# Optimization experiments

Hardware: AMD Instinct MI355X
Metric: run time of the kernel (lower is better)

Reference implementation:

```python
import jax, jax.numpy as jnp
import numpy as np

B, C, H, W = 8, 320, 32, 32
HEADS, DHEAD = 8, 40
CTX_LEN, CTX_DIM = 77, 768
FF_INNER = 4 * C
GROUPS = 32
HW = H * W


def setup_inputs() -> dict:
    key = jax.random.key(0)
    ks = jax.random.split(key, 16)
    def nrm(k, shape, s=0.02):
        return (jax.random.normal(k, shape) * s).astype(jnp.float32)
    z = lambda *s: jnp.zeros(s, jnp.float32)
    o = lambda *s: jnp.ones(s, jnp.float32)
    inp = {}
    inp["x"] = jax.random.normal(ks[0], (B, C, H, W), jnp.float32)
    inp["context"] = jax.random.normal(ks[1], (B, CTX_LEN, CTX_DIM), jnp.float32)
    inp["vis_mask"] = jax.random.uniform(ks[2], (B, HW, HW)) > 0.5
    inp["v2t_mask"] = jax.random.uniform(ks[3], (B, HW, CTX_LEN)) > 0.5
    inp["gn_scale"] = o(C); inp["gn_bias"] = z(C)
    inp["proj_in_w"] = nrm(ks[4], (C, C)); inp["proj_in_b"] = z(C)
    inp["n1_s"] = o(C); inp["n1_b"] = z(C)
    inp["wq1"] = nrm(ks[5], (C, C)); inp["wk1"] = nrm(ks[6], (C, C)); inp["wv1"] = nrm(ks[7], (C, C))
    inp["wo1"] = nrm(ks[8], (C, C)); inp["bo1"] = z(C)
    inp["n2_s"] = o(C); inp["n2_b"] = z(C)
    inp["wq2"] = nrm(ks[9], (C, C)); inp["wk2"] = nrm(ks[10], (CTX_DIM, C)); inp["wv2"] = nrm(ks[11], (CTX_DIM, C))
    inp["wo2"] = nrm(ks[12], (C, C)); inp["bo2"] = z(C)
    inp["n3_s"] = o(C); inp["n3_b"] = z(C)
    inp["ff_w1"] = nrm(ks[13], (C, 2 * FF_INNER)); inp["ff_b1"] = z(2 * FF_INNER)
    inp["ff_w2"] = nrm(ks[14], (FF_INNER, C)); inp["ff_b2"] = z(C)
    inp["proj_out_w"] = nrm(ks[15], (C, C)); inp["proj_out_b"] = z(C)
    return inp


def group_norm(x, scale, bias, eps=1e-6):
    b, c, h, w = x.shape
    xg = x.reshape(b, GROUPS, -1)
    mu = xg.mean(-1, keepdims=True)
    var = xg.var(-1, keepdims=True)
    xn = ((xg - mu) * jax.lax.rsqrt(var + eps)).reshape(b, c, h, w)
    return xn * scale[None, :, None, None] + bias[None, :, None, None]


def layer_norm(x, s, b, eps=1e-5):
    mu = x.mean(-1, keepdims=True)
    var = x.var(-1, keepdims=True)
    return (x - mu) * jax.lax.rsqrt(var + eps) * s + b


def mha(xq, ctx, wq, wk, wv, wo, bo, mask):
    # CrossAttention: manual einsum softmax with boolean mask broadcast over heads
    b, n, _ = xq.shape
    m = ctx.shape[1]
    split = lambda t: t.reshape(b, -1, HEADS, DHEAD).transpose(0, 2, 1, 3)
    q = split(xq @ wq)   # [b,h,n,d]
    k = split(ctx @ wk)  # [b,h,m,d]
    v = split(ctx @ wv)
    sim = jnp.einsum('bhid,bhjd->bhij', q, k) * (DHEAD ** -0.5)
    if mask is not None:
        sim = jnp.where(mask[:, None, :, :], sim, jnp.finfo(sim.dtype).min)
    attn = jax.nn.softmax(sim, axis=-1)
    out = jnp.einsum('bhij,bhjd->bhid', attn, v)
    out = out.transpose(0, 2, 1, 3).reshape(b, n, HEADS * DHEAD)
    return out @ wo + bo


def reference(x, context, vis_mask, v2t_mask, gn_scale, gn_bias, proj_in_w, proj_in_b,
              n1_s, n1_b, wq1, wk1, wv1, wo1, bo1,
              n2_s, n2_b, wq2, wk2, wv2, wo2, bo2,
              n3_s, n3_b, ff_w1, ff_b1, ff_w2, ff_b2,
              proj_out_w, proj_out_b):
    x_in = x
    h = group_norm(x, gn_scale, gn_bias)
    # 1x1 conv proj_in == per-pixel linear; flatten b c h w -> b (hw) c
    h = h.reshape(B, C, HW).transpose(0, 2, 1) @ proj_in_w + proj_in_b
    # masked self-attention (vis mask)
    h = h + mha(layer_norm(h, n1_s, n1_b), layer_norm(h, n1_s, n1_b),
                wq1, wk1, wv1, wo1, bo1, vis_mask)
    # masked cross-attention to text (v2t mask)
    h = h + mha(layer_norm(h, n2_s, n2_b), context,
                wq2, wk2, wv2, wo2, bo2, v2t_mask)
    # GEGLU feedforward (glu=True, mult=4)
    y = layer_norm(h, n3_s, n3_b) @ ff_w1 + ff_b1
    a, g = jnp.split(y, 2, axis=-1)
    h = h + (a * jax.nn.gelu(g, approximate=False)) @ ff_w2 + ff_b2
    # proj_out + residual
    out = (h @ proj_out_w + proj_out_b).transpose(0, 2, 1).reshape(B, C, H, W)
    return out + x_in
```

## Files before the change

kernel.cpp:

```cpp
#include <hip/hip_runtime.h>
#include <hip/hip_bf16.h>
#include <math.h>


#define Bsz   8
#define Cch   320
#define HW    1024
#define NTOK  (Bsz*HW)
#define HEADS 8
#define DHEAD 40
#define CTXL  77
#define CTXD  768
#define FFI   1280
#define MCTX  (Bsz*CTXL)
#define MCTXP 640

typedef unsigned short u16;
typedef unsigned long long u64;
typedef __attribute__((ext_vector_type(8))) u16    u16x8;
typedef __attribute__((ext_vector_type(8))) __bf16 bf16x8;
typedef __attribute__((ext_vector_type(4))) float  f32x4;

__device__ inline u16 f2b(float f) {
    unsigned u = __float_as_uint(f);
    return (u16)((u + 0x7FFFu + ((u >> 16) & 1u)) >> 16);
}

__global__ __launch_bounds__(256) void gn_apply(
    const float* __restrict__ x, const float* __restrict__ gnA,
    const float* __restrict__ gnB, u16* __restrict__ out)
{
    __shared__ u16 T[64*72];
    const int tid = threadIdx.x;
    const int c0 = blockIdx.x * 64;
    const int p0 = blockIdx.y * 64;
    const int b  = blockIdx.z;
    for (int e = tid; e < 512; e += 256) {
        int r = e >> 3, ch = e & 7;
        const float* src = x + ((size_t)(b*Cch + c0 + r))*HW + p0 + ch*8;
        float a  = gnA[b*Cch + c0 + r];
        float bb = gnB[b*Cch + c0 + r];
        float4 v0 = *(const float4*)src;
        float4 v1 = *(const float4*)(src + 4);
        u16x8 val;
        val[0] = f2b(v0.x*a + bb); val[1] = f2b(v0.y*a + bb);
        val[2] = f2b(v0.z*a + bb); val[3] = f2b(v0.w*a + bb);
        val[4] = f2b(v1.x*a + bb); val[5] = f2b(v1.y*a + bb);
        val[6] = f2b(v1.z*a + bb); val[7] = f2b(v1.w*a + bb);
        *(u16x8*)&T[r*72 + (ch ^ (r & 7))*8] = val;
    }
    __syncthreads();
    for (int e = tid; e < 4096; e += 256) {
        int p = e >> 6, c = e & 63;
        u16 v = T[c*72 + (((p >> 3) ^ (c & 7))*8) + (p & 7)];
        out[((size_t)(b*HW + p0 + p))*Cch + c0 + c] = v;
    }
}

__global__ __launch_bounds__(256) void layernorm_kernel(
    const float* __restrict__ in, const float* __restrict__ s,
    const float* __restrict__ bgain, u16* __restrict__ out)
{
    int t = blockIdx.x*4 + (threadIdx.x >> 6);
    int lane = threadIdx.x & 63;
    const float* row = in + (size_t)t*Cch;
    float v[5];
    float sum = 0.f, sq = 0.f;
    #pragma unroll
    for (int i = 0; i < 5; ++i) {
        v[i] = row[lane + 64*i];
        sum += v[i]; sq += v[i]*v[i];
    }
    #pragma unroll
    for (int off = 32; off > 0; off >>= 1) {
        sum += __shfl_xor(sum, off);
        sq  += __shfl_xor(sq,  off);
    }
    float mean = sum * (1.f/320.f);
    float var  = sq  * (1.f/320.f) - mean*mean;
    float inv  = rsqrtf(var + 1e-5f);
    u16* orow = out + (size_t)t*Cch;
    #pragma unroll
    for (int i = 0; i < 5; ++i) {
        int c = lane + 64*i;
        orow[c] = f2b((v[i]-mean)*inv*s[c] + bgain[c]);
    }
}

struct WDesc { const float* src; u16* dst; int K; int N; int tiles; float scl; };
struct WPack { WDesc w[12]; };

#define WT_TILES 620
#define CTXBLK   240

__global__ __launch_bounds__(256) void preamble(
    WPack p, const float* __restrict__ ctxsrc, u16* __restrict__ ctxdst,
    const void* __restrict__ vis, const void* __restrict__ v2t,
    u64* __restrict__ bvis, u64* __restrict__ bv2t,
    const float* __restrict__ x, const float* __restrict__ gscale,
    const float* __restrict__ gbias, float* __restrict__ gnA,
    float* __restrict__ gnB)
{
    __shared__ u16 T[64*72];
    int blk = blockIdx.x;
    int tid = threadIdx.x;
    if (blk < WT_TILES) {
        int t = blk;
        #pragma unroll
        for (int i = 0; i < 12; ++i) {
            int nt = p.w[i].tiles;
            if (t < nt) {
                const int K = p.w[i].K, N = p.w[i].N;
                const int ntN = N >> 6;
                const int tk = t / ntN, tn = t - tk*ntN;
                const float scl = p.w[i].scl;
                const float* src = p.w[i].src;
                u16* dst = p.w[i].dst;
                for (int e = tid; e < 512; e += 256) {
                    int r = e >> 3, ch = e & 7;
                    const float* sp = src + (size_t)(tk*64 + r)*N + tn*64 + ch*8;
                    float4 v0 = *(const float4*)sp;
                    float4 v1 = *(const float4*)(sp + 4);
                    u16x8 val;
                    val[0] = f2b(v0.x*scl); val[1] = f2b(v0.y*scl);
                    val[2] = f2b(v0.z*scl); val[3] = f2b(v0.w*scl);
                    val[4] = f2b(v1.x*scl); val[5] = f2b(v1.y*scl);
                    val[6] = f2b(v1.z*scl); val[7] = f2b(v1.w*scl);
                    *(u16x8*)&T[r*72 + (ch ^ (r & 7))*8] = val;
                }
                __syncthreads();
                for (int e = tid; e < 4096; e += 256) {
                    int n = e >> 6, k = e & 63;
                    u16 v = T[k*72 + (((n >> 3) ^ (k & 7))*8) + (n & 7)];
                    dst[(size_t)(tn*64 + n)*K + tk*64 + k] = v;
                }
                return;
            }
            t -= nt;
        }
        return;
    }
    if (blk < WT_TILES + CTXBLK) {
        int idx = (blk - WT_TILES)*2048 + tid*8;
        int r = idx / CTXD;
        u16x8 val = {};
        if (r < MCTX) {
            float4 v0 = *(const float4*)(ctxsrc + idx);
            float4 v1 = *(const float4*)(ctxsrc + idx + 4);
            val[0] = f2b(v0.x); val[1] = f2b(v0.y);
            val[2] = f2b(v0.z); val[3] = f2b(v0.w);
            val[4] = f2b(v1.x); val[5] = f2b(v1.y);
            val[6] = f2b(v1.z); val[7] = f2b(v1.w);
        }
        *(u16x8*)(ctxdst + idx) = val;
        return;
    }
    if (blk >= WT_TILES + CTXBLK + 4096) {
        int gb = blk - (WT_TILES + CTXBLK + 4096);
        int b = gb >> 5, g = gb & 31;
        __shared__ float rs[256], rq[256];
        const float4* xg = (const float4*)(x + ((size_t)b*Cch + g*10)*HW);
        float s = 0.f, q = 0.f;
        #pragma unroll
        for (int i = 0; i < 10; ++i) {
            float4 v = xg[tid + i*256];
            s += v.x + v.y + v.z + v.w;
            q += v.x*v.x + v.y*v.y + v.z*v.z + v.w*v.w;
        }
        rs[tid] = s; rq[tid] = q; __syncthreads();
        for (int off = 128; off > 0; off >>= 1) {
            if (tid < off) { rs[tid] += rs[tid+off]; rq[tid] += rq[tid+off]; }
            __syncthreads();
        }
        if (tid < 10) {
            float mean = rs[0] * (1.f/10240.f);
            float var  = rq[0] * (1.f/10240.f) - mean*mean;
            float inv  = rsqrtf(var + 1e-6f);
            int chn = g*10 + tid;
            float a = inv * gscale[chn];
            gnA[b*Cch + chn] = a;
            gnB[b*Cch + chn] = gbias[chn] - mean*a;
        }
        return;
    }
    __shared__ int any;
    if (tid == 0) any = 0;
    __syncthreads();
    const unsigned char* probe = (const unsigned char*)vis;
    for (int i = tid; i < 4096; i += 256)
        if ((i & 3) && probe[i]) any = 1;
    __syncthreads();
    const int isU8 = any;
    int mb = blk - WT_TILES - CTXBLK;
    const void* mask; u64* bits; int Lkv, nw;
    if (mb < 2048) { mask = vis; bits = bvis; Lkv = HW;   nw = 16; }
    else           { mask = v2t; bits = bv2t; Lkv = CTXL; nw = 2; mb -= 2048; }
    const int wv = tid >> 6, lane = tid & 63;
    const int row = mb*4 + wv;
    const unsigned char* m8  = (const unsigned char*)mask;
    const int*           m32 = (const int*)mask;
    const size_t base = (size_t)row * Lkv;
    for (int w = 0; w < nw; ++w) {
        int j = w*64 + lane;
        bool on = (j < Lkv) && (isU8 ? (m8[base+j] != 0) : (m32[base+j] != 0));
        u64 word = __ballot(on);
        if (lane == 0) bits[(size_t)row*nw + w] = word;
    }
}

__global__ __launch_bounds__(512) void gemm_bf16(
    const u16* __restrict__ A, const u16* __restrict__ Wt,
    const float* __restrict__ bias, const float* __restrict__ res,
    float* __restrict__ out, u16* __restrict__ out_bf, int M, int N, int K)
{
    __shared__ u16 As[2][128*40];
    __shared__ u16 Bs[2][64*40];
    const int tid  = threadIdx.x;
    const int lane = tid & 63;
    const int w    = tid >> 6;
    const int mp   = w >> 1;
    const int np   = w & 1;
    const int m0   = blockIdx.y * 128;
    const int n0   = blockIdx.x * 64;
    const int fr   = lane & 15, fg = lane >> 4;
    const int ar   = tid >> 2, ac = tid & 3;
    const bool hasB = tid < 256;

    const u16* pa = A  + (size_t)(m0 + ar)*K + ac*8;
    const u16* pb = Wt + (size_t)(n0 + ar)*K + ac*8;
    const int nk = K >> 5;

    *(u16x8*)&As[0][ar*40 + ac*8] = *(const u16x8*)pa;
    if (hasB) *(u16x8*)&Bs[0][ar*40 + ac*8] = *(const u16x8*)pb;
    u16x8 xa = *(const u16x8*)(pa + 32);
    u16x8 ya = *(const u16x8*)(pa + 64);
    u16x8 xb = {}, yb = {};
    if (hasB) { xb = *(const u16x8*)(pb + 32); yb = *(const u16x8*)(pb + 64); }

    f32x4 acc[2][2] = {};
    for (int i = 0; i < nk; i += 2) {
        __syncthreads();
        *(u16x8*)&As[1][ar*40 + ac*8] = xa;
        if (hasB) *(u16x8*)&Bs[1][ar*40 + ac*8] = xb;
        if (i + 3 < nk) {
            xa = *(const u16x8*)(pa + 32*(i+3));
            if (hasB) xb = *(const u16x8*)(pb + 32*(i+3));
        }
        {
            bf16x8 a0 = *(const bf16x8*)&As[0][(mp*32      + fr)*40 + fg*8];
            bf16x8 a1 = *(const bf16x8*)&As[0][(mp*32 + 16 + fr)*40 + fg*8];
            #pragma unroll
            for (int t = 0; t < 2; ++t) {
                bf16x8 b = *(const bf16x8*)&Bs[0][((np*2+t)*16 + fr)*40 + fg*8];
                acc[0][t] = __builtin_amdgcn_mfma_f32_16x16x32_bf16(a0, b, acc[0][t], 0, 0, 0);
                acc[1][t] = __builtin_amdgcn_mfma_f32_16x16x32_bf16(a1, b, acc[1][t], 0, 0, 0);
            }
        }
        __syncthreads();
        if (i + 2 < nk) {
            *(u16x8*)&As[0][ar*40 + ac*8] = ya;
            if (hasB) *(u16x8*)&Bs[0][ar*40 + ac*8] = yb;
            if (i + 4 < nk) {
                ya = *(const u16x8*)(pa + 32*(i+4));
                if (hasB) yb = *(const u16x8*)(pb + 32*(i+4));
            }
        }
        {
            bf16x8 a0 = *(const bf16x8*)&As[1][(mp*32      + fr)*40 + fg*8];
            bf16x8 a1 = *(const bf16x8*)&As[1][(mp*32 + 16 + fr)*40 + fg*8];
            #pragma unroll
            for (int t = 0; t < 2; ++t) {
                bf16x8 b = *(const bf16x8*)&Bs[1][((np*2+t)*16 + fr)*40 + fg*8];
                acc[0][t] = __builtin_amdgcn_mfma_f32_16x16x32_bf16(a0, b, acc[0][t], 0, 0, 0);
                acc[1][t] = __builtin_amdgcn_mfma_f32_16x16x32_bf16(a1, b, acc[1][t], 0, 0, 0);
            }
        }
    }
    #pragma unroll
    for (int at = 0; at < 2; ++at) {
        #pragma unroll
        for (int t = 0; t < 2; ++t) {
            int gn = n0 + (np*2+t)*16 + fr;
            float bv = bias ? bias[gn] : 0.f;
            #pragma unroll
            for (int i = 0; i < 4; ++i) {
                int gm = m0 + mp*32 + at*16 + fg*4 + i;
                float v = acc[at][t][i] + bv;
                if (res) v += res[(size_t)gm*N + gn];
                if (out) out[(size_t)gm*N + gn] = v;
                if (out_bf) out_bf[(size_t)gm*N + gn] = f2b(v);
            }
        }
    }
}

__global__ __launch_bounds__(512) void gemm_pout(
    const u16* __restrict__ A, const u16* __restrict__ Wt,
    const float* __restrict__ bias, const float* __restrict__ x,
    float* __restrict__ out, int K)
{
    __shared__ u16 As[2][128*40];
    __shared__ u16 Bs[2][64*40];
    const int tid  = threadIdx.x;
    const int lane = tid & 63;
    const int w    = tid >> 6;
    const int mp   = w >> 1;
    const int np   = w & 1;
    const int m0   = blockIdx.y * 128;
    const int n0   = blockIdx.x * 64;
    const int fr   = lane & 15, fg = lane >> 4;
    const int ar   = tid >> 2, ac = tid & 3;
    const bool hasB = tid < 256;

    const u16* pa = A  + (size_t)(m0 + ar)*K + ac*8;
    const u16* pb = Wt + (size_t)(n0 + ar)*K + ac*8;
    const int nk = K >> 5;

    *(u16x8*)&As[0][ar*40 + ac*8] = *(const u16x8*)pa;
    if (hasB) *(u16x8*)&Bs[0][ar*40 + ac*8] = *(const u16x8*)pb;
    u16x8 xa = *(const u16x8*)(pa + 32);
    u16x8 ya = *(const u16x8*)(pa + 64);
    u16x8 xb = {}, yb = {};
    if (hasB) { xb = *(const u16x8*)(pb + 32); yb = *(const u16x8*)(pb + 64); }

    f32x4 acc[2][2] = {};
    for (int i = 0; i < nk; i += 2) {
        __syncthreads();
        *(u16x8*)&As[1][ar*40 + ac*8] = xa;
        if (hasB) *(u16x8*)&Bs[1][ar*40 + ac*8] = xb;
        if (i + 3 < nk) {
            xa = *(const u16x8*)(pa + 32*(i+3));
            if (hasB) xb = *(const u16x8*)(pb + 32*(i+3));
        }
        {
            bf16x8 a0 = *(const bf16x8*)&As[0][(mp*32      + fr)*40 + fg*8];
            bf16x8 a1 = *(const bf16x8*)&As[0][(mp*32 + 16 + fr)*40 + fg*8];
            #pragma unroll
            for (int t = 0; t < 2; ++t) {
                bf16x8 b = *(const bf16x8*)&Bs[0][((np*2+t)*16 + fr)*40 + fg*8];
                acc[0][t] = __builtin_amdgcn_mfma_f32_16x16x32_bf16(a0, b, acc[0][t], 0, 0, 0);
                acc[1][t] = __builtin_amdgcn_mfma_f32_16x16x32_bf16(a1, b, acc[1][t], 0, 0, 0);
            }
        }
        __syncthreads();
        if (i + 2 < nk) {
            *(u16x8*)&As[0][ar*40 + ac*8] = ya;
            if (hasB) *(u16x8*)&Bs[0][ar*40 + ac*8] = yb;
            if (i + 4 < nk) {
                ya = *(const u16x8*)(pa + 32*(i+4));
                if (hasB) yb = *(const u16x8*)(pb + 32*(i+4));
            }
        }
        {
            bf16x8 a0 = *(const bf16x8*)&As[1][(mp*32      + fr)*40 + fg*8];
            bf16x8 a1 = *(const bf16x8*)&As[1][(mp*32 + 16 + fr)*40 + fg*8];
            #pragma unroll
            for (int t = 0; t < 2; ++t) {
                bf16x8 b = *(const bf16x8*)&Bs[1][((np*2+t)*16 + fr)*40 + fg*8];
                acc[0][t] = __builtin_amdgcn_mfma_f32_16x16x32_bf16(a0, b, acc[0][t], 0, 0, 0);
                acc[1][t] = __builtin_amdgcn_mfma_f32_16x16x32_bf16(a1, b, acc[1][t], 0, 0, 0);
            }
        }
    }
    #pragma unroll
    for (int at = 0; at < 2; ++at) {
        #pragma unroll
        for (int t = 0; t < 2; ++t) {
            int gn = n0 + (np*2+t)*16 + fr;
            float bv = bias[gn];
            int gm0 = m0 + mp*32 + at*16 + fg*4;
            int b   = gm0 >> 10;
            int pcol= gm0 & (HW-1);
            size_t o = ((size_t)(b*Cch + gn))*HW + pcol;
            f32x4 xv = *(const f32x4*)&x[o];
            f32x4 vv;
            #pragma unroll
            for (int i = 0; i < 4; ++i) vv[i] = acc[at][t][i] + bv + xv[i];
            *(f32x4*)&out[o] = vv;
        }
    }
}

__global__ __launch_bounds__(512) void ctx_kv_gemm(
    const u16* __restrict__ ctx, const u16* __restrict__ wk,
    const u16* __restrict__ wv, u16* __restrict__ kout, u16* __restrict__ vout)
{
    __shared__ u16 As[2][64*40];
    __shared__ u16 Bs[2][64*40];
    const int tid  = threadIdx.x;
    const int lane = tid & 63;
    const int w    = tid >> 6;
    const int mg   = w >> 1;
    const int np   = w & 1;
    const int m0   = blockIdx.y * 64;
    const int n0   = blockIdx.x * 64;
    const u16* Wt  = blockIdx.z ? wv : wk;
    u16* outp      = blockIdx.z ? vout : kout;
    const int fr   = lane & 15, fg = lane >> 4;
    const bool isA = tid < 256;
    const int cr   = (tid & 255) >> 2, cc = tid & 3;

    const u16* ps = isA ? ctx + (size_t)(m0 + cr)*CTXD + cc*8
                        : Wt  + (size_t)(n0 + cr)*CTXD + cc*8;
    u16* s0 = isA ? &As[0][cr*40 + cc*8] : &Bs[0][cr*40 + cc*8];
    u16* s1 = isA ? &As[1][cr*40 + cc*8] : &Bs[1][cr*40 + cc*8];
    const int nk = CTXD >> 5;

    *(u16x8*)s0 = *(const u16x8*)ps;
    u16x8 xv = *(const u16x8*)(ps + 32);
    u16x8 yv = *(const u16x8*)(ps + 64);

    f32x4 acc[2] = {};
    for (int i = 0; i < nk; i += 2) {
        __syncthreads();
        *(u16x8*)s1 = xv;
        if (i + 3 < nk) xv = *(const u16x8*)(ps + 32*(i+3));
        {
            bf16x8 a = *(const bf16x8*)&As[0][(mg*16 + fr)*40 + fg*8];
            #pragma unroll
            for (int t = 0; t < 2; ++t) {
                bf16x8 b = *(const bf16x8*)&Bs[0][((np*2+t)*16 + fr)*40 + fg*8];
                acc[t] = __builtin_amdgcn_mfma_f32_16x16x32_bf16(a, b, acc[t], 0, 0, 0);
            }
        }
        __syncthreads();
        if (i + 2 < nk) {
            *(u16x8*)s0 = yv;
            if (i + 4 < nk) yv = *(const u16x8*)(ps + 32*(i+4));
        }
        {
            bf16x8 a = *(const bf16x8*)&As[1][(mg*16 + fr)*40 + fg*8];
            #pragma unroll
            for (int t = 0; t < 2; ++t) {
                bf16x8 b = *(const bf16x8*)&Bs[1][((np*2+t)*16 + fr)*40 + fg*8];
                acc[t] = __builtin_amdgcn_mfma_f32_16x16x32_bf16(a, b, acc[t], 0, 0, 0);
            }
        }
    }
    #pragma unroll
    for (int t = 0; t < 2; ++t) {
        int gn = n0 + (np*2+t)*16 + fr;
        #pragma unroll
        for (int i = 0; i < 4; ++i) {
            int gm = m0 + mg*16 + fg*4 + i;
            if (gm < MCTX)
                outp[(size_t)gm*Cch + gn] = f2b(acc[t][i]);
        }
    }
}

__global__ __launch_bounds__(512) void geglu_bf16(
    const u16* __restrict__ A, const u16* __restrict__ Wt,
    const float* __restrict__ b1, u16* __restrict__ out, int M, int K)
{
    __shared__ u16 As[2][128*40];
    __shared__ u16 Ba[2][64*40];
    __shared__ u16 Bg[2][64*40];
    const int tid  = threadIdx.x;
    const int lane = tid & 63;
    const int w    = tid >> 6;
    const int mp   = w >> 1;
    const int np   = w & 1;
    const int m0   = blockIdx.y * 128;
    const int n0   = blockIdx.x * 64;
    const int fr   = lane & 15, fg = lane >> 4;
    const int ar   = tid >> 2, ac = tid & 3;
    const int nk   = K >> 5;

    const u16* pa = A + (size_t)(m0 + ar)*K + ac*8;
    const int bq = (ar < 64) ? (n0 + ar) : (FFI + n0 + ar - 64);
    const u16* pb = Wt + (size_t)bq*K + ac*8;
    u16* bs0 = (ar < 64) ? &Ba[0][ar*40 + ac*8] : &Bg[0][(ar-64)*40 + ac*8];
    u16* bs1 = (ar < 64) ? &Ba[1][ar*40 + ac*8] : &Bg[1][(ar-64)*40 + ac*8];

    *(u16x8*)&As[0][ar*40 + ac*8] = *(const u16x8*)pa;
    *(u16x8*)bs0 = *(const u16x8*)pb;
    u16x8 xa = *(const u16x8*)(pa + 32);
    u16x8 xb = *(const u16x8*)(pb + 32);
    u16x8 ya = *(const u16x8*)(pa + 64);
    u16x8 yb = *(const u16x8*)(pb + 64);

    f32x4 aca[2][2] = {}, acg[2][2] = {};
    for (int i = 0; i < nk; i += 2) {
        __syncthreads();
        *(u16x8*)&As[1][ar*40 + ac*8] = xa;
        *(u16x8*)bs1 = xb;
        if (i + 3 < nk) {
            xa = *(const u16x8*)(pa + 32*(i+3));
            xb = *(const u16x8*)(pb + 32*(i+3));
        }
        {
            bf16x8 a0 = *(const bf16x8*)&As[0][(mp*32      + fr)*40 + fg*8];
            bf16x8 a1 = *(const bf16x8*)&As[0][(mp*32 + 16 + fr)*40 + fg*8];
            #pragma unroll
            for (int t = 0; t < 2; ++t) {
                bf16x8 ba = *(const bf16x8*)&Ba[0][((np*2+t)*16 + fr)*40 + fg*8];
                bf16x8 bg = *(const bf16x8*)&Bg[0][((np*2+t)*16 + fr)*40 + fg*8];
                aca[0][t] = __builtin_amdgcn_mfma_f32_16x16x32_bf16(a0, ba, aca[0][t], 0, 0, 0);
                aca[1][t] = __builtin_amdgcn_mfma_f32_16x16x32_bf16(a1, ba, aca[1][t], 0, 0, 0);
                acg[0][t] = __builtin_amdgcn_mfma_f32_16x16x32_bf16(a0, bg, acg[0][t], 0, 0, 0);
                acg[1][t] = __builtin_amdgcn_mfma_f32_16x16x32_bf16(a1, bg, acg[1][t], 0, 0, 0);
            }
        }
        __syncthreads();
        if (i + 2 < nk) {
            *(u16x8*)&As[0][ar*40 + ac*8] = ya;
            *(u16x8*)bs0 = yb;
            if (i + 4 < nk) {
                ya = *(const u16x8*)(pa + 32*(i+4));
                yb = *(const u16x8*)(pb + 32*(i+4));
            }
        }
        {
            bf16x8 a0 = *(const bf16x8*)&As[1][(mp*32      + fr)*40 + fg*8];
            bf16x8 a1 = *(const bf16x8*)&As[1][(mp*32 + 16 + fr)*40 + fg*8];
            #pragma unroll
            for (int t = 0; t < 2; ++t) {
                bf16x8 ba = *(const bf16x8*)&Ba[1][((np*2+t)*16 + fr)*40 + fg*8];
                bf16x8 bg = *(const bf16x8*)&Bg[1][((np*2+t)*16 + fr)*40 + fg*8];
                aca[0][t] = __builtin_amdgcn_mfma_f32_16x16x32_bf16(a0, ba, aca[0][t], 0, 0, 0);
                aca[1][t] = __builtin_amdgcn_mfma_f32_16x16x32_bf16(a1, ba, aca[1][t], 0, 0, 0);
                acg[0][t] = __builtin_amdgcn_mfma_f32_16x16x32_bf16(a0, bg, acg[0][t], 0, 0, 0);
                acg[1][t] = __builtin_amdgcn_mfma_f32_16x16x32_bf16(a1, bg, acg[1][t], 0, 0, 0);
            }
        }
    }
    #pragma unroll
    for (int at = 0; at < 2; ++at) {
        #pragma unroll
        for (int t = 0; t < 2; ++t) {
            int gn = n0 + (np*2+t)*16 + fr;
            float ba = b1[gn], bg = b1[FFI + gn];
            #pragma unroll
            for (int i = 0; i < 4; ++i) {
                int gm = m0 + mp*32 + at*16 + fg*4 + i;
                float av = aca[at][t][i] + ba;
                float gv = acg[at][t][i] + bg;
                float gel = 0.5f*gv*(1.f + erff(gv*0.70710678118654752f));
                out[(size_t)gm*FFI + gn] = f2b(av*gel);
            }
        }
    }
}

__global__ __launch_bounds__(256) void transpose_v(
    const u16* __restrict__ in, int istride, u16* __restrict__ out,
    int Ltok, int ostride)
{
    __shared__ u16 T[64*72];
    const int tid = threadIdx.x;
    const int c0 = blockIdx.x * 64;
    const int t0 = blockIdx.y * 64;
    const int b  = blockIdx.z;
    for (int e = tid; e < 512; e += 256) {
        int r = e >> 3, ch = e & 7;
        u16x8 val = {};
        if (t0 + r < Ltok)
            val = *(const u16x8*)(in + ((size_t)(b*Ltok + t0 + r))*istride + c0 + ch*8);
        *(u16x8*)&T[r*72 + (ch ^ (r & 7))*8] = val;
    }
    __syncthreads();
    for (int e = tid; e < 4096; e += 256) {
        int c = e >> 6, t = e & 63;
        u16 v = T[t*72 + (((c >> 3) ^ (t & 7))*8) + (c & 7)];
        out[((size_t)(b*Cch + c0 + c))*ostride + t0 + t] = v;
    }
}

__global__ __launch_bounds__(256) void flash_mfma(
    const u16* __restrict__ qb, int qstride,
    const u16* __restrict__ kb, int kstride,
    const u16* __restrict__ vt, int vstride,
    const u64* __restrict__ mbits, int nw,
    u16* __restrict__ out,
    int Lkv)
{
    __shared__ u16 QPs[64*72];
    __shared__ u16 Ks[64*72];
    __shared__ u16 Vs[48*72];

    const int tid  = threadIdx.x;
    const int lane = tid & 63;
    const int w    = tid >> 6;
    const int col  = lane & 15;
    const int quad = lane >> 4;
    const int q0   = blockIdx.x * 64;
    const int h    = blockIdx.y;
    const int b    = blockIdx.z;
    const int ch   = tid & 7;
    const int r0   = tid >> 3;

    {
        const u16* qT = qb + ((size_t)(b*HW + q0))*qstride + (size_t)h*DHEAD + ch*8;
        u16x8 v0 = {}, v1 = {};
        if (ch < 5) {
            v0 = *(const u16x8*)(qT + (size_t)r0*qstride);
            v1 = *(const u16x8*)(qT + (size_t)(r0+32)*qstride);
        }
        *(u16x8*)&QPs[r0*72 + ch*8]      = v0;
        *(u16x8*)&QPs[(r0+32)*72 + ch*8] = v1;
    }
    if (tid >= 64 && tid < 128) {
        int dc = 32 + (tid >> 3);
        u16x8 v = {};
        if (dc == DHEAD) {
            #pragma unroll
            for (int z = 0; z < 8; ++z) v[z] = 0x3F80;
        }
        *(u16x8*)&Vs[dc*72 + ch*8] = v;
    }

    const bool kok = ch < 5;
    const u16* kR0 = kb + (size_t)b*Lkv*kstride + (size_t)h*DHEAD + ch*8
                        + (size_t)r0*kstride;
    const u16* kR1 = kR0 + (size_t)32*kstride;
    const int d1   = 32 + (tid >> 3);
    const u16* vR0 = vt + ((size_t)(b*Cch + h*DHEAD))*vstride + ch*8
                        + (size_t)r0*vstride;
    const u16* vR1 = vt + ((size_t)(b*Cch + h*DHEAD))*vstride + ch*8
                        + (size_t)d1*vstride;
    const u64* mrow = mbits + ((size_t)(b*HW + q0 + w*16 + quad*4))*nw;
    const bool vok1 = tid < 64;

    u16x8 nk0 = {}, nk1 = {}, nv0, nv1 = {};
    if (kok && (r0      < Lkv)) nk0 = *(const u16x8*)kR0;
    if (kok && (r0 + 32 < Lkv)) nk1 = *(const u16x8*)kR1;
    nv0 = *(const u16x8*)vR0;
    if (vok1) nv1 = *(const u16x8*)vR1;

    __syncthreads();
    const bf16x8 qa0 = *(const bf16x8*)&QPs[(w*16 + col)*72 +  0 + quad*8];
    const bf16x8 qa1 = *(const bf16x8*)&QPs[(w*16 + col)*72 + 32 + quad*8];

    f32x4 acc_o[3] = {};

    const int nkt = (Lkv + 63) / 64;
    for (int jt = 0; jt < nkt; ++jt) {
        __syncthreads();
        *(u16x8*)&Ks[r0*72 + ch*8]      = nk0;
        *(u16x8*)&Ks[(r0+32)*72 + ch*8] = nk1;
        *(u16x8*)&Vs[r0*72 + ch*8]      = nv0;
        if (vok1) *(u16x8*)&Vs[d1*72 + ch*8] = nv1;
        if (jt + 1 < nkt) {
            const int j0n = (jt + 1)*64;
            kR0 += (size_t)64*kstride;
            kR1 += (size_t)64*kstride;
            vR0 += 64; vR1 += 64;
            nk0 = (u16x8){}; nk1 = (u16x8){};
            if (kok && (j0n + r0      < Lkv)) nk0 = *(const u16x8*)kR0;
            if (kok && (j0n + r0 + 32 < Lkv)) nk1 = *(const u16x8*)kR1;
            nv0 = *(const u16x8*)vR0;
            if (vok1) nv1 = *(const u16x8*)vR1;
        }
        __syncthreads();

        u64 mw[4];
        #pragma unroll
        for (int i = 0; i < 4; ++i) mw[i] = mrow[i*nw + jt];

        f32x4 s[4] = {};
        #pragma unroll
        for (int nt = 0; nt < 4; ++nt) {
            bf16x8 b0 = *(const bf16x8*)&Ks[(nt*16 + col)*72 +  0 + quad*8];
            bf16x8 b1 = *(const bf16x8*)&Ks[(nt*16 + col)*72 + 32 + quad*8];
            s[nt] = __builtin_amdgcn_mfma_f32_16x16x32_bf16(qa0, b0, s[nt], 0, 0, 0);
            s[nt] = __builtin_amdgcn_mfma_f32_16x16x32_bf16(qa1, b1, s[nt], 0, 0, 0);
        }

        #pragma unroll
        for (int i = 0; i < 4; ++i) {
            #pragma unroll
            for (int nt = 0; nt < 4; ++nt) {
                float p = __builtin_amdgcn_exp2f(s[nt][i]);
                unsigned bits = (unsigned)(mw[i] >> (nt*16));
                s[nt][i] = ((bits >> col) & 1u) ? p : 0.f;
            }
        }

        #pragma unroll
        for (int nt = 0; nt < 4; ++nt)
            #pragma unroll
            for (int i = 0; i < 4; ++i)
                QPs[(w*16 + quad*4 + i)*68 + nt*16 + col] =
                    (u16)(__float_as_uint(s[nt][i]) >> 16);

        bf16x8 pa0, pa1;
        __builtin_memcpy(&pa0, &QPs[(w*16 + col)*68 +  0 + quad*8], 16);
        __builtin_memcpy(&pa1, &QPs[(w*16 + col)*68 + 32 + quad*8], 16);
        #pragma unroll
        for (int nt = 0; nt < 3; ++nt) {
            bf16x8 vb0 = *(const bf16x8*)&Vs[(nt*16 + col)*72 +  0 + quad*8];
            bf16x8 vb1 = *(const bf16x8*)&Vs[(nt*16 + col)*72 + 32 + quad*8];
            acc_o[nt] = __builtin_amdgcn_mfma_f32_16x16x32_bf16(pa0, vb0, acc_o[nt], 0, 0, 0);
            acc_o[nt] = __builtin_amdgcn_mfma_f32_16x16x32_bf16(pa1, vb1, acc_o[nt], 0, 0, 0);
        }
    }

    float inv_l[4];
    #pragma unroll
    for (int i = 0; i < 4; ++i)
        inv_l[i] = 1.f / __shfl(acc_o[2][i], (lane & 48) | 8);

    #pragma unroll
    for (int nt = 0; nt < 3; ++nt) {
        int d = nt*16 + col;
        if (d < DHEAD) {
            #pragma unroll
            for (int i = 0; i < 4; ++i) {
                int q = q0 + w*16 + quad*4 + i;
                out[((size_t)(b*HW + q))*Cch + h*DHEAD + d] = f2b(acc_o[nt][i] * inv_l[i]);
            }
        }
    }
}

extern "C" void kernel_launch(void* const* d_in, const int* in_sizes, int n_in,
                              void* d_out, int out_size, void* d_ws, size_t ws_size,
                              hipStream_t stream)
{
    const float* x        = (const float*)d_in[0];
    const float* context  = (const float*)d_in[1];
    const void*  vis_mask = d_in[2];
    const void*  v2t_mask = d_in[3];
    const float* gn_s     = (const float*)d_in[4];
    const float* gn_b     = (const float*)d_in[5];
    const float* proj_in_w= (const float*)d_in[6];
    const float* proj_in_b= (const float*)d_in[7];
    const float* n1_s     = (const float*)d_in[8];
    const float* n1_b     = (const float*)d_in[9];
    const float* wq1      = (const float*)d_in[10];
    const float* wk1      = (const float*)d_in[11];
    const float* wv1      = (const float*)d_in[12];
    const float* wo1      = (const float*)d_in[13];
    const float* bo1      = (const float*)d_in[14];
    const float* n2_s     = (const float*)d_in[15];
    const float* n2_b     = (const float*)d_in[16];
    const float* wq2      = (const float*)d_in[17];
    const float* wk2      = (const float*)d_in[18];
    const float* wv2      = (const float*)d_in[19];
    const float* wo2      = (const float*)d_in[20];
    const float* bo2      = (const float*)d_in[21];
    const float* n3_s     = (const float*)d_in[22];
    const float* n3_b     = (const float*)d_in[23];
    const float* ff_w1    = (const float*)d_in[24];
    const float* ff_b1    = (const float*)d_in[25];
    const float* ff_w2    = (const float*)d_in[26];
    const float* ff_b2    = (const float*)d_in[27];
    const float* pout_w   = (const float*)d_in[28];
    const float* pout_b   = (const float*)d_in[29];
    float* out = (float*)d_out;

    const size_t TOKC = (size_t)NTOK*Cch;
    float* ws   = (float*)d_ws;
    float* Hb   = ws;
    u16*   QKV  = (u16*)(Hb + TOKC);
    u16*   Vt_g = QKV + 3*TOKC;
    u16*   G_bf = QKV;
    u16*   T0b  = Vt_g + TOKC;
    u16*   T1b  = T0b + TOKC;
    u16*   Hb_bf= T1b + TOKC;
    u16*   Wbf  = Hb_bf + TOKC;
    u64*   mb_vis = (u64*)(Wbf + 2539520);
    u64*   mb_v2t = mb_vis + 131072;
    u16*   ctx_bf = (u16*)(mb_v2t + 16384);
    u16*   Kc_bf  = ctx_bf + MCTXP*CTXD;
    u16*   Vc_bf  = Kc_bf + 640*Cch;
    float* gnA    = (float*)(Vc_bf + 640*Cch);
    float* gnB    = gnA + Bsz*Cch;

    u16* w_q1  = Wbf;
    u16* w_k1  = Wbf +  102400;
    u16* w_v1  = Wbf +  204800;
    u16* w_pin = Wbf +  307200;
    u16* w_o1  = Wbf +  409600;
    u16* w_q2  = Wbf +  512000;
    u16* w_o2  = Wbf +  614400;
    u16* w_ff1 = Wbf +  716800;
    u16* w_ff2 = Wbf + 1536000;
    u16* w_po  = Wbf + 1945600;
    u16* w_k2  = Wbf + 2048000;
    u16* w_v2  = Wbf + 2293760;

    const float qscale = 0.15811388300841897f * 1.4426950408889634f;
    WPack pack;
    pack.w[0]  = { wq1,       w_q1,  Cch, Cch, 25,  qscale };
    pack.w[1]  = { wk1,       w_k1,  Cch, Cch, 25,  1.f };
    pack.w[2]  = { wv1,       w_v1,  Cch, Cch, 25,  1.f };
    pack.w[3]  = { proj_in_w, w_pin, Cch, Cch, 25,  1.f };
    pack.w[4]  = { wo1,       w_o1,  Cch, Cch, 25,  1.f };
    pack.w[5]  = { wq2,       w_q2,  Cch, Cch, 25,  qscale };
    pack.w[6]  = { wo2,       w_o2,  Cch, Cch, 25,  1.f };
    pack.w[7]  = { ff_w1,     w_ff1, Cch, 2*FFI, 200, 1.f };
    pack.w[8]  = { ff_w2,     w_ff2, FFI, Cch, 100, 1.f };
    pack.w[9]  = { pout_w,    w_po,  Cch, Cch, 25,  1.f };
    pack.w[10] = { wk2,       w_k2,  CTXD, Cch, 60, 1.f };
    pack.w[11] = { wv2,       w_v2,  CTXD, Cch, 60, 1.f };

    dim3 blk256(256);
    dim3 blk512(512);
    dim3 gTok(Cch/64, NTOK/128);
    dim3 gQKV(960/64, NTOK/128);
    dim3 gKV(Cch/64, MCTXP/64, 2);
    dim3 gFF(FFI/64, NTOK/128);
    dim3 gFA(HW/64, HEADS, Bsz);
    dim3 gTrS(Cch/64, HW/64, Bsz);
    dim3 gTrX(Cch/64, 2, Bsz);
    dim3 gGN(Cch/64, HW/64, Bsz);

    preamble<<<WT_TILES + CTXBLK + 4096 + 256, blk256, 0, stream>>>(
        pack, context, ctx_bf, vis_mask, v2t_mask, mb_vis, mb_v2t,
        x, gn_s, gn_b, gnA, gnB);

    gn_apply<<<gGN, blk256, 0, stream>>>(x, gnA, gnB, T0b);
    gemm_bf16<<<gTok, blk512, 0, stream>>>(T0b, w_pin, proj_in_b, nullptr, Hb, nullptr, NTOK, Cch, Cch);

    layernorm_kernel<<<NTOK/4, blk256, 0, stream>>>(Hb, n1_s, n1_b, T0b);
    gemm_bf16<<<gQKV, blk512, 0, stream>>>(T0b, w_q1, nullptr, nullptr, nullptr, QKV, NTOK, 960, Cch);
    transpose_v<<<gTrS, blk256, 0, stream>>>(QKV + 640, 960, Vt_g, HW, HW);
    flash_mfma<<<gFA, blk256, 0, stream>>>(QKV, 960, QKV + 320, 960, Vt_g, HW,
                                           mb_vis, 16, T1b, HW);
    gemm_bf16<<<gTok, blk512, 0, stream>>>(T1b, w_o1, bo1, Hb, Hb, nullptr, NTOK, Cch, Cch);

    layernorm_kernel<<<NTOK/4, blk256, 0, stream>>>(Hb, n2_s, n2_b, T0b);
    gemm_bf16<<<gTok, blk512, 0, stream>>>(T0b, w_q2, nullptr, nullptr, nullptr, QKV, NTOK, Cch, Cch);
    ctx_kv_gemm<<<gKV, blk512, 0, stream>>>(ctx_bf, w_k2, w_v2, Kc_bf, Vc_bf);
    transpose_v<<<gTrX, blk256, 0, stream>>>(Vc_bf, Cch, Vt_g, CTXL, 128);
    flash_mfma<<<gFA, blk256, 0, stream>>>(QKV, Cch, Kc_bf, Cch, Vt_g, 128,
                                           mb_v2t, 2, T1b, CTXL);
    gemm_bf16<<<gTok, blk512, 0, stream>>>(T1b, w_o2, bo2, Hb, Hb, nullptr, NTOK, Cch, Cch);

    layernorm_kernel<<<NTOK/4, blk256, 0, stream>>>(Hb, n3_s, n3_b, T0b);
    geglu_bf16<<<gFF, blk512, 0, stream>>>(T0b, w_ff1, ff_b1, G_bf, NTOK, Cch);
    gemm_bf16<<<gTok, blk512, 0, stream>>>(G_bf, w_ff2, ff_b2, Hb, nullptr, Hb_bf, NTOK, Cch, FFI);

    gemm_pout<<<gTok, blk512, 0, stream>>>(Hb_bf, w_po, pout_b, x, out, Cch);
}
```

Before: 377.8 us.

## Widen flash attention tile to 128 queries with double-buffered K/V

The flash attention kernel now runs 512-thread blocks that each handle 128 query rows instead of 64. Each staged K/V tile is therefore shared by twice as many queries, halving K/V global loads per query. K and V shared-memory buffers are double-buffered, so each iteration needs one barrier instead of two. A flat 1-D grid with a swizzled mapping to (batch, head, query tile) replaces the 3-D grid, probably for cache locality. In exchange, shared memory per block roughly doubles and there are half as many blocks, which may reduce occupancy and latency hiding.

```diff
diff --git a/kernel.cpp b/kernel.cpp
--- a/kernel.cpp
+++ b/kernel.cpp
@@ -567,7 +567,7 @@
     }
 }
 
-__global__ __launch_bounds__(256) void flash_mfma(
+__global__ __launch_bounds__(512) void flash_mfma(
     const u16* __restrict__ qb, int qstride,
     const u16* __restrict__ kb, int kstride,
     const u16* __restrict__ vt, int vstride,
@@ -575,18 +575,21 @@
     u16* __restrict__ out,
     int Lkv)
 {
-    __shared__ u16 QPs[64*72];
-    __shared__ u16 Ks[64*72];
-    __shared__ u16 Vs[48*72];
+    __shared__ u16 QPs[128*72];
+    __shared__ u16 Ks[2][64*72];
+    __shared__ u16 Vs[2][48*72];
 
     const int tid  = threadIdx.x;
     const int lane = tid & 63;
     const int w    = tid >> 6;
     const int col  = lane & 15;
     const int quad = lane >> 4;
-    const int q0   = blockIdx.x * 64;
-    const int h    = blockIdx.y;
-    const int b    = blockIdx.z;
+    const int bi   = blockIdx.x;
+    const int hb   = (bi & 7)*8 + (bi >> 6);
+    const int qt   = (bi >> 3) & 7;
+    const int h    = hb & 7;
+    const int b    = hb >> 3;
+    const int q0   = qt*128;
     const int ch   = tid & 7;
     const int r0   = tid >> 3;
 
@@ -595,38 +598,34 @@
         u16x8 v0 = {}, v1 = {};
         if (ch < 5) {
             v0 = *(const u16x8*)(qT + (size_t)r0*qstride);
-            v1 = *(const u16x8*)(qT + (size_t)(r0+32)*qstride);
+            v1 = *(const u16x8*)(qT + (size_t)(r0+64)*qstride);
         }
         *(u16x8*)&QPs[r0*72 + ch*8]      = v0;
-        *(u16x8*)&QPs[(r0+32)*72 + ch*8] = v1;
-    }
-    if (tid >= 64 && tid < 128) {
-        int dc = 32 + (tid >> 3);
+        *(u16x8*)&QPs[(r0+64)*72 + ch*8] = v1;
+    }
+    if (tid < 128) {
+        int rr  = tid >> 3;
+        int row = 40 + (rr & 7);
+        int buf = rr >> 3;
         u16x8 v = {};
-        if (dc == DHEAD) {
+        if (row == DHEAD) {
             #pragma unroll
             for (int z = 0; z < 8; ++z) v[z] = 0x3F80;
         }
-        *(u16x8*)&Vs[dc*72 + ch*8] = v;
+        *(u16x8*)&Vs[buf][row*72 + ch*8] = v;
     }
 
     const bool kok = ch < 5;
-    const u16* kR0 = kb + (size_t)b*Lkv*kstride + (size_t)h*DHEAD + ch*8
-                        + (size_t)r0*kstride;
-    const u16* kR1 = kR0 + (size_t)32*kstride;
-    const int d1   = 32 + (tid >> 3);
-    const u16* vR0 = vt + ((size_t)(b*Cch + h*DHEAD))*vstride + ch*8
-                        + (size_t)r0*vstride;
-    const u16* vR1 = vt + ((size_t)(b*Cch + h*DHEAD))*vstride + ch*8
-                        + (size_t)d1*vstride;
+    const u16* kR = kb + (size_t)b*Lkv*kstride + (size_t)h*DHEAD + ch*8
+                       + (size_t)r0*kstride;
+    const u16* vR = vt + ((size_t)(b*Cch + h*DHEAD))*vstride + ch*8
+                       + (size_t)r0*vstride;
+    const bool vok = r0 < DHEAD;
     const u64* mrow = mbits + ((size_t)(b*HW + q0 + w*16 + quad*4))*nw;
-    const bool vok1 = tid < 64;
-
-    u16x8 nk0 = {}, nk1 = {}, nv0, nv1 = {};
-    if (kok && (r0      < Lkv)) nk0 = *(const u16x8*)kR0;
-    if (kok && (r0 + 32 < Lkv)) nk1 = *(const u16x8*)kR1;
-    nv0 = *(const u16x8*)vR0;
-    if (vok1) nv1 = *(const u16x8*)vR1;
+
+    u16x8 nk = {}, nv = {};
+    if (kok && r0 < Lkv) nk = *(const u16x8*)kR;
+    if (vok) nv = *(const u16x8*)vR;
 
     __syncthreads();
     const bf16x8 qa0 = *(const bf16x8*)&QPs[(w*16 + col)*72 +  0 + quad*8];
@@ -635,24 +634,18 @@
     f32x4 acc_o[3] = {};
 
     const int nkt = (Lkv + 63) / 64;
+    int cur = 0;
     for (int jt = 0; jt < nkt; ++jt) {
+        *(u16x8*)&Ks[cur][r0*72 + ch*8] = nk;
+        if (vok) *(u16x8*)&Vs[cur][r0*72 + ch*8] = nv;
+        if (jt + 1 < nkt) {
+            kR += (size_t)64*kstride;
+            vR += 64;
+            nk = (u16x8){};
+            if (kok && ((jt+1)*64 + r0 < Lkv)) nk = *(const u16x8*)kR;
+            if (vok) nv = *(const u16x8*)vR;
+        }
         __syncthreads();
-        *(u16x8*)&Ks[r0*72 + ch*8]      = nk0;
-        *(u16x8*)&Ks[(r0+32)*72 + ch*8] = nk1;
-        *(u16x8*)&Vs[r0*72 + ch*8]      = nv0;
-        if (vok1) *(u16x8*)&Vs[d1*72 + ch*8] = nv1;
-        if (jt + 1 < nkt) {
-            const int j0n = (jt + 1)*64;
-            kR0 += (size_t)64*kstride;
-            kR1 += (size_t)64*kstride;
-            vR0 += 64; vR1 += 64;
-            nk0 = (u16x8){}; nk1 = (u16x8){};
-            if (kok && (j0n + r0      < Lkv)) nk0 = *(const u16x8*)kR0;
-            if (kok && (j0n + r0 + 32 < Lkv)) nk1 = *(const u16x8*)kR1;
-            nv0 = *(const u16x8*)vR0;
-            if (vok1) nv1 = *(const u16x8*)vR1;
-        }
-        __syncthreads();
 
         u64 mw[4];
         #pragma unroll
@@ -661,8 +654,8 @@
         f32x4 s[4] = {};
         #pragma unroll
         for (int nt = 0; nt < 4; ++nt) {
-            bf16x8 b0 = *(const bf16x8*)&Ks[(nt*16 + col)*72 +  0 + quad*8];
-            bf16x8 b1 = *(const bf16x8*)&Ks[(nt*16 + col)*72 + 32 + quad*8];
+            bf16x8 b0 = *(const bf16x8*)&Ks[cur][(nt*16 + col)*72 +  0 + quad*8];
+            bf16x8 b1 = *(const bf16x8*)&Ks[cur][(nt*16 + col)*72 + 32 + quad*8];
             s[nt] = __builtin_amdgcn_mfma_f32_16x16x32_bf16(qa0, b0, s[nt], 0, 0, 0);
             s[nt] = __builtin_amdgcn_mfma_f32_16x16x32_bf16(qa1, b1, s[nt], 0, 0, 0);
         }
@@ -689,11 +682,12 @@
         __builtin_memcpy(&pa1, &QPs[(w*16 + col)*68 + 32 + quad*8], 16);
         #pragma unroll
         for (int nt = 0; nt < 3; ++nt) {
-            bf16x8 vb0 = *(const bf16x8*)&Vs[(nt*16 + col)*72 +  0 + quad*8];
-            bf16x8 vb1 = *(const bf16x8*)&Vs[(nt*16 + col)*72 + 32 + quad*8];
+            bf16x8 vb0 = *(const bf16x8*)&Vs[cur][(nt*16 + col)*72 +  0 + quad*8];
+            bf16x8 vb1 = *(const bf16x8*)&Vs[cur][(nt*16 + col)*72 + 32 + quad*8];
             acc_o[nt] = __builtin_amdgcn_mfma_f32_16x16x32_bf16(pa0, vb0, acc_o[nt], 0, 0, 0);
             acc_o[nt] = __builtin_amdgcn_mfma_f32_16x16x32_bf16(pa1, vb1, acc_o[nt], 0, 0, 0);
         }
+        cur ^= 1;
     }
 
     float inv_l[4];
@@ -802,7 +796,6 @@
     dim3 gQKV(960/64, NTOK/128);
     dim3 gKV(Cch/64, MCTXP/64, 2);
     dim3 gFF(FFI/64, NTOK/128);
-    dim3 gFA(HW/64, HEADS, Bsz);
     dim3 gTrS(Cch/64, HW/64, Bsz);
     dim3 gTrX(Cch/64, 2, Bsz);
     dim3 gGN(Cch/64, HW/64, Bsz);
@@ -817,7 +810,7 @@
     layernorm_kernel<<<NTOK/4, blk256, 0, stream>>>(Hb, n1_s, n1_b, T0b);
     gemm_bf16<<<gQKV, blk512, 0, stream>>>(T0b, w_q1, nullptr, nullptr, nullptr, QKV, NTOK, 960, Cch);
     transpose_v<<<gTrS, blk256, 0, stream>>>(QKV + 640, 960, Vt_g, HW, HW);
-    flash_mfma<<<gFA, blk256, 0, stream>>>(QKV, 960, QKV + 320, 960, Vt_g, HW,
+    flash_mfma<<<512, blk512, 0, stream>>>(QKV, 960, QKV + 320, 960, Vt_g, HW,
                                            mb_vis, 16, T1b, HW);
     gemm_bf16<<<gTok, blk512, 0, stream>>>(T1b, w_o1, bo1, Hb, Hb, nullptr, NTOK, Cch, Cch);
 
@@ -825,7 +818,7 @@
     gemm_bf16<<<gTok, blk512, 0, stream>>>(T0b, w_q2, nullptr, nullptr, nullptr, QKV, NTOK, Cch, Cch);
     ctx_kv_gemm<<<gKV, blk512, 0, stream>>>(ctx_bf, w_k2, w_v2, Kc_bf, Vc_bf);
     transpose_v<<<gTrX, blk256, 0, stream>>>(Vc_bf, Cch, Vt_g, CTXL, 128);
-    flash_mfma<<<gFA, blk256, 0, stream>>>(QKV, Cch, Kc_bf, Cch, Vt_g, 128,
+    flash_mfma<<<512, blk512, 0, stream>>>(QKV, Cch, Kc_bf, Cch, Vt_g, 128,
                                            mb_v2t, 2, T1b, CTXL);
     gemm_bf16<<<gTok, blk512, 0, stream>>>(T1b, w_o2, bo2, Hb, Hb, nullptr, NTOK, Cch, Cch);
 
```

Result: no change. 375.9 us (-0.5%).
